# Optimization experiments

Measured on AMD Instinct MI355X. Metric: run time of the kernel, lower is better.

## Reference

```python
import jax, jax.numpy as jnp
import numpy as np

N, E, D, H, O, G = 50000, 800000, 64, 64, 32, 64


def setup_inputs() -> dict:
    key = jax.random.key(0)
    ks = jax.random.split(key, 12)
    x = jax.random.normal(ks[0], (N, D), dtype=jnp.float32)
    edge_index = jax.random.randint(ks[1], (2, E), 0, N)
    batch = jnp.sort(jax.random.randint(ks[2], (N,), 0, G))

    def glorot(k, fan_in, fan_out):
        s = np.sqrt(6.0 / (fan_in + fan_out)).astype(np.float32)
        return jax.random.uniform(k, (fan_in, fan_out), jnp.float32, -s, s)

    return {
        "x": x,
        "edge_index": edge_index,
        "batch": batch,
        "W1": glorot(ks[3], D, H), "b1": jnp.zeros((H,), jnp.float32),
        "W2": glorot(ks[4], H, H), "b2": jnp.zeros((H,), jnp.float32),
        "W3": glorot(ks[5], H, H), "b3": jnp.zeros((H,), jnp.float32),
        "Wl": glorot(ks[6], H, O), "bl": jnp.zeros((O,), jnp.float32),
    }


def reference(x, edge_index, batch, W1, b1, W2, b2, W3, b3, Wl, bl):
    n = x.shape[0]
    # GCNConv default: add self-loops, symmetric deg^-1/2 normalization
    loop = jnp.arange(n, dtype=edge_index.dtype)
    src = jnp.concatenate([edge_index[0], loop])  # [E+N]
    dst = jnp.concatenate([edge_index[1], loop])
    deg = jax.ops.segment_sum(jnp.ones_like(src, dtype=x.dtype), dst, num_segments=n)
    dis = jax.lax.rsqrt(deg)  # deg >= 1 due to self-loops
    norm = (dis[src] * dis[dst])[:, None]  # [E+N, 1]

    def gcn(h, W, b):
        hw = h @ W                      # [N, H] small GEMM
        msg = hw[src] * norm            # gather + scale: [E+N, H]
        agg = jax.ops.segment_sum(msg, dst, num_segments=n)  # scatter-add
        return agg + b

    h = jax.nn.relu(gcn(x, W1, b1))
    h = jax.nn.relu(gcn(h, W2, b2))
    h = gcn(h, W3, b3)

    # global_mean_pool over graph ids
    counts = jax.ops.segment_sum(jnp.ones((n,), h.dtype), batch, num_segments=G)
    pooled = jax.ops.segment_sum(h, batch, num_segments=G) / counts[:, None]

    # dropout(p=0.5) is identity in eval mode
    return pooled @ Wl + bl
```

## Files before the change

kernel.cpp:

```cpp
#include <hip/hip_runtime.h>

#define HD 64
#define PSUB 16
#define NBLK 256
#define LOG_NBLK 8
#define NBKT 512

__device__ __forceinline__ unsigned short f2bf(float f) {
    union { float f; unsigned u; } v; v.f = f;
    unsigned r = v.u + 0x7FFF + ((v.u >> 16) & 1);
    return (unsigned short)(r >> 16);
}
__device__ __forceinline__ float u2f(unsigned u) {
    union { unsigned u; float f; } v; v.u = u;
    return v.f;
}


__global__ __launch_bounds__(256) void hist1_k(const int* __restrict__ dst,
                                               int* __restrict__ hist, int E, int chunk)
{
    __shared__ int lh[NBKT];
    int t = threadIdx.x;
    for (int i = t; i < NBKT; i += 256) lh[i] = 0;
    __syncthreads();
    int base = blockIdx.x * chunk;
    int end  = min(base + chunk, E);
    for (int i = base + t; i < end; i += 256)
        atomicAdd(&lh[dst[i] >> 7], 1);
    __syncthreads();
    for (int i = t; i < NBKT; i += 256)
        hist[blockIdx.x * NBKT + i] = lh[i];
}

__global__ __launch_bounds__(256) void scanA_k(const int* __restrict__ hist,
                                               int* __restrict__ tsum)
{
    __shared__ int s[256];
    int t = threadIdx.x;
    int l = blockIdx.x * 256 + t;
    int phys = (l & (NBLK - 1)) * NBKT + (l >> LOG_NBLK);
    s[t] = hist[phys];
    __syncthreads();
    for (int off = 128; off > 0; off >>= 1) {
        if (t < off) s[t] += s[t + off];
        __syncthreads();
    }
    if (t == 0) tsum[blockIdx.x] = s[0];
}

__global__ __launch_bounds__(1024) void scanB_k(int* __restrict__ tsum, int nb,
    const int* __restrict__ batch, int* __restrict__ gstart, int n, int G,
    float* __restrict__ partial, int psz)
{
    __shared__ int s[1024];
    int t = threadIdx.x;
    int v = (t < nb) ? tsum[t] : 0;
    s[t] = v;
    __syncthreads();
    for (int off = 1; off < 1024; off <<= 1) {
        int u = (t >= off) ? s[t - off] : 0;
        __syncthreads();
        s[t] += u;
        __syncthreads();
    }
    if (t < nb) tsum[t] = s[t] - v;
    if (t <= G) {
        if (t == G) gstart[t] = n;
        else {
            int lo = 0, hi = n;
            while (lo < hi) { int m = (lo + hi) >> 1; if (batch[m] < t) lo = m + 1; else hi = m; }
            gstart[t] = lo;
        }
    }
    for (int i = t; i < psz; i += 1024) partial[i] = 0.f;
}

__global__ __launch_bounds__(256) void scanC_k(const int* __restrict__ hist,
                                               const int* __restrict__ tsum,
                                               int* __restrict__ scanned)
{
    __shared__ int s[256];
    int t = threadIdx.x;
    int l = blockIdx.x * 256 + t;
    int phys = (l & (NBLK - 1)) * NBKT + (l >> LOG_NBLK);
    int own = hist[phys];
    s[t] = own;
    __syncthreads();
    for (int off = 1; off < 256; off <<= 1) {
        int u = (t >= off) ? s[t - off] : 0;
        __syncthreads();
        s[t] += u;
        __syncthreads();
    }
    scanned[l] = tsum[blockIdx.x] + s[t] - own;
}

__global__ __launch_bounds__(256) void append_k(const int* __restrict__ src,
    const int* __restrict__ dst, const int* __restrict__ scanned,
    int* __restrict__ pairs, int E, int chunk)
{
    __shared__ int cur[NBKT];
    int t = threadIdx.x;
    int blk = blockIdx.x;
    for (int i = t; i < NBKT; i += 256) cur[i] = scanned[i * NBLK + blk];
    __syncthreads();
    int base = blk * chunk;
    int end  = min(base + chunk, E);
    for (int i = base + t; i < end; i += 256) {
        int s = src[i], d = dst[i];
        int p = atomicAdd(&cur[d >> 7], 1);
        pairs[p] = (s << 7) | (d & 127);
    }
}

__global__ __launch_bounds__(256) void bucket_csr_k(const int* __restrict__ pairs,
    const int* __restrict__ scanned, int* __restrict__ offsets,
    float* __restrict__ dis, int* __restrict__ csr_src, int N, int E)
{
    __shared__ int cnt[128];
    __shared__ int sc[128];
    __shared__ int cur[128];
    int t = threadIdx.x;
    int b = blockIdx.x;
    int nodeBase = b * 128;
    int nNodes = min(128, N - nodeBase);
    int bBase = scanned[b * NBLK];
    int bEnd  = (b + 1 < NBKT) ? scanned[(b + 1) * NBLK] : E;

    if (t < 128) cnt[t] = 0;
    __syncthreads();
    for (int i = bBase + t; i < bEnd; i += 256)
        atomicAdd(&cnt[pairs[i] & 127], 1);
    __syncthreads();
    int myc = (t < 128) ? cnt[t] : 0;
    if (t < 128) sc[t] = myc;
    __syncthreads();
    for (int off = 1; off < 128; off <<= 1) {
        int u = (t < 128 && t >= off) ? sc[t - off] : 0;
        __syncthreads();
        if (t < 128) sc[t] += u;
        __syncthreads();
    }
    if (t < 128) {
        int excl = sc[t] - myc;
        cur[t] = excl;
        if (t < nNodes) {
            offsets[nodeBase + t] = bBase + excl;
            dis[nodeBase + t] = rsqrtf(1.0f + (float)myc);
        }
    }
    if (t == 0 && b == gridDim.x - 1) offsets[N] = E;
    __syncthreads();
    for (int i = bBase + t; i < bEnd; i += 256) {
        int pk = pairs[i];
        int pos = bBase + atomicAdd(&cur[pk & 127], 1);
        csr_src[pos] = ((unsigned)pk) >> 7;
    }
}


__global__ __launch_bounds__(256) void gemm64_k(
    const float* __restrict__ in, const float* __restrict__ b_prev, int relu_prev,
    const float* __restrict__ W, const float* __restrict__ dis,
    unsigned short* __restrict__ outb, int n)
{
    __shared__ float HsT[HD][68];
    __shared__ float Ws[HD][HD];
    int t = threadIdx.x;
    int rowBase = blockIdx.x * 64;

    for (int i = t; i < HD * HD / 4; i += 256)
        ((float4*)Ws)[i] = ((const float4*)W)[i];

    if (blockIdx.x == 0 && t < 64)
        outb[(size_t)n * HD + t] = 0;

    {
        int k0 = (t & 15) * 4;
        float4 bb = make_float4(0.f, 0.f, 0.f, 0.f);
        if (b_prev) bb = *(const float4*)&b_prev[k0];
        for (int it = 0; it < 4; ++it) {
            int r = (t >> 4) + it * 16;
            int row = rowBase + r;
            float4 v = make_float4(0.f, 0.f, 0.f, 0.f);
            if (row < n) {
                v = *(const float4*)&in[(size_t)row * HD + k0];
                v.x += bb.x; v.y += bb.y; v.z += bb.z; v.w += bb.w;
                if (relu_prev) {
                    v.x = fmaxf(v.x, 0.f); v.y = fmaxf(v.y, 0.f);
                    v.z = fmaxf(v.z, 0.f); v.w = fmaxf(v.w, 0.f);
                }
            }
            HsT[k0 + 0][r] = v.x;
            HsT[k0 + 1][r] = v.y;
            HsT[k0 + 2][r] = v.z;
            HsT[k0 + 3][r] = v.w;
        }
    }
    __syncthreads();

    int c4 = (t & 15) * 4;
    int r4 = (t >> 4) * 4;
    float acc[4][4];
    #pragma unroll
    for (int i = 0; i < 4; ++i)
        #pragma unroll
        for (int j = 0; j < 4; ++j) acc[i][j] = 0.f;

    #pragma unroll 8
    for (int k = 0; k < HD; ++k) {
        float4 a = *(const float4*)&HsT[k][r4];
        float4 b = *(const float4*)&Ws[k][c4];
        acc[0][0] += a.x * b.x; acc[0][1] += a.x * b.y; acc[0][2] += a.x * b.z; acc[0][3] += a.x * b.w;
        acc[1][0] += a.y * b.x; acc[1][1] += a.y * b.y; acc[1][2] += a.y * b.z; acc[1][3] += a.y * b.w;
        acc[2][0] += a.z * b.x; acc[2][1] += a.z * b.y; acc[2][2] += a.z * b.z; acc[2][3] += a.z * b.w;
        acc[3][0] += a.w * b.x; acc[3][1] += a.w * b.y; acc[3][2] += a.w * b.z; acc[3][3] += a.w * b.w;
    }

    #pragma unroll
    for (int i = 0; i < 4; ++i) {
        int row = rowBase + r4 + i;
        if (row < n) {
            float ds = dis[row];
            ushort4 o;
            o.x = f2bf(ds * acc[i][0]); o.y = f2bf(ds * acc[i][1]);
            o.z = f2bf(ds * acc[i][2]); o.w = f2bf(ds * acc[i][3]);
            *(ushort4*)&outb[(size_t)row * HD + c4] = o;
        }
    }
}

__device__ __forceinline__ void gather4(const unsigned short* __restrict__ hwb,
    const int* __restrict__ offsets, const int* __restrict__ csr_src,
    int node, bool act, int n, int sub, int fl,
    float& a0, float& a1, float& a2, float& a3)
{
    int beg = 0, end = 0;
    if (act) { beg = offsets[node]; end = offsets[node + 1]; }
    int deg = end - beg;
    int md = deg;
    md = max(md, __shfl_xor(md, 16, 64));
    md = max(md, __shfl_xor(md, 32, 64));

    int nodeC = act ? node : n;
    uint2 sv = *(const uint2*)(hwb + ((size_t)nodeC << 6) + (fl << 2));
    a0 = u2f(sv.x << 16); a1 = u2f(sv.x & 0xFFFF0000u);
    a2 = u2f(sv.y << 16); a3 = u2f(sv.y & 0xFFFF0000u);

    int base = sub << 4;
    for (int jb = 0; jb < md; jb += 16) {
        int e = jb + fl;
        int idxv = (e < deg) ? csr_src[beg + e] : n;
        {
            uint2 g[8];
            #pragma unroll
            for (int j = 0; j < 8; ++j) {
                int row = __shfl(idxv, base + j, 64);
                g[j] = *(const uint2*)(hwb + ((size_t)row << 6) + (fl << 2));
            }
            #pragma unroll
            for (int j = 0; j < 8; ++j) {
                a0 += u2f(g[j].x << 16); a1 += u2f(g[j].x & 0xFFFF0000u);
                a2 += u2f(g[j].y << 16); a3 += u2f(g[j].y & 0xFFFF0000u);
            }
        }
        if (jb + 8 < md) {
            uint2 g[8];
            #pragma unroll
            for (int j = 0; j < 8; ++j) {
                int row = __shfl(idxv, base + 8 + j, 64);
                g[j] = *(const uint2*)(hwb + ((size_t)row << 6) + (fl << 2));
            }
            #pragma unroll
            for (int j = 0; j < 8; ++j) {
                a0 += u2f(g[j].x << 16); a1 += u2f(g[j].x & 0xFFFF0000u);
                a2 += u2f(g[j].y << 16); a3 += u2f(g[j].y & 0xFFFF0000u);
            }
        }
    }
}

__global__ __launch_bounds__(256) void agg4_k(const unsigned short* __restrict__ hwb,
    const float* __restrict__ dis, const int* __restrict__ offsets,
    const int* __restrict__ csr_src, float* __restrict__ agg, int n)
{
    int t    = threadIdx.x;
    int lane = t & 63;
    int sub  = lane >> 4;
    int fl   = lane & 15;
    int node = blockIdx.x * 16 + (t >> 6) * 4 + sub;
    bool act = node < n;

    float a0, a1, a2, a3;
    gather4(hwb, offsets, csr_src, node, act, n, sub, fl, a0, a1, a2, a3);

    if (act) {
        float ds = dis[node];
        *(float4*)&agg[(size_t)node * HD + (fl << 2)] =
            make_float4(a0 * ds, a1 * ds, a2 * ds, a3 * ds);
    }
}

__global__ __launch_bounds__(256) void agg_pool4_k(const unsigned short* __restrict__ hwb,
    const float* __restrict__ dis, const int* __restrict__ offsets,
    const int* __restrict__ csr_src, const int* __restrict__ batch,
    float* __restrict__ partial, int n)
{
    __shared__ float sh[16][68];
    __shared__ int gids[16];
    __shared__ int allsame;
    int t    = threadIdx.x;
    int lane = t & 63;
    int sub  = lane >> 4;
    int fl   = lane & 15;
    int w    = t >> 6;
    int nib  = w * 4 + sub;
    int node = blockIdx.x * 16 + nib;
    bool act = node < n;

    float a0, a1, a2, a3;
    gather4(hwb, offsets, csr_src, node, act, n, sub, fl, a0, a1, a2, a3);

    float ds = act ? dis[node] : 0.f;
    *(float4*)&sh[nib][fl << 2] = make_float4(a0 * ds, a1 * ds, a2 * ds, a3 * ds);
    if (fl == 0) gids[nib] = act ? batch[node] : -1;
    __syncthreads();

    if (t == 0) {
        int g0 = gids[0];
        int ok = (g0 >= 0);
        #pragma unroll
        for (int r = 1; r < 16; ++r) ok &= (gids[r] == g0);
        allsame = ok;
    }
    __syncthreads();

    int slot = blockIdx.x & (PSUB - 1);
    if (allsame) {
        if (t < 64) {
            float s = 0.f;
            #pragma unroll
            for (int r = 0; r < 16; ++r) s += sh[r][t];
            atomicAdd(&partial[((size_t)gids[0] * PSUB + slot) * HD + t], s);
        }
    } else {
        int c  = t & 63;
        int r0 = w * 4;
        int ga = gids[r0], gb = gids[r0 + 1], gc = gids[r0 + 2], gd = gids[r0 + 3];
        if (ga == gb && gb == gc && gc == gd && ga >= 0) {
            float v = sh[r0][c] + sh[r0 + 1][c] + sh[r0 + 2][c] + sh[r0 + 3][c];
            atomicAdd(&partial[((size_t)ga * PSUB + slot) * HD + c], v);
        } else {
            if (ga >= 0) atomicAdd(&partial[((size_t)ga * PSUB + slot) * HD + c], sh[r0][c]);
            if (gb >= 0) atomicAdd(&partial[((size_t)gb * PSUB + slot) * HD + c], sh[r0 + 1][c]);
            if (gc >= 0) atomicAdd(&partial[((size_t)gc * PSUB + slot) * HD + c], sh[r0 + 2][c]);
            if (gd >= 0) atomicAdd(&partial[((size_t)gd * PSUB + slot) * HD + c], sh[r0 + 3][c]);
        }
    }
}

__global__ __launch_bounds__(64) void pool2_k(const float* __restrict__ partial,
    const int* __restrict__ gstart, const float* __restrict__ b3,
    const float* __restrict__ Wl, const float* __restrict__ bl,
    float* __restrict__ out, int O)
{
    __shared__ float pooled[HD];
    int g = blockIdx.x;
    int t = threadIdx.x;
    float sum = 0.0f;
    #pragma unroll
    for (int s = 0; s < PSUB; ++s)
        sum += partial[((size_t)g * PSUB + s) * HD + t];
    float cnt = (float)(gstart[g + 1] - gstart[g]);
    pooled[t] = sum / cnt + b3[t];
    __syncthreads();
    if (t < O) {
        float acc = bl[t];
        #pragma unroll
        for (int k = 0; k < HD; ++k) acc += pooled[k] * Wl[k * O + t];
        out[g * O + t] = acc;
    }
}

extern "C" void kernel_launch(void* const* d_in, const int* in_sizes, int n_in,
                              void* d_out, int out_size, void* d_ws, size_t ws_size,
                              hipStream_t stream)
{
    const float* x    = (const float*)d_in[0];
    const int*   ei   = (const int*)d_in[1];
    const int*   batch= (const int*)d_in[2];
    const float* W1   = (const float*)d_in[3];
    const float* b1   = (const float*)d_in[4];
    const float* W2   = (const float*)d_in[5];
    const float* b2   = (const float*)d_in[6];
    const float* W3   = (const float*)d_in[7];
    const float* b3   = (const float*)d_in[8];
    const float* Wl   = (const float*)d_in[9];
    const float* bl   = (const float*)d_in[10];
    float* out = (float*)d_out;

    const int N = in_sizes[0] / HD;
    const int E = in_sizes[1] / 2;
    const int O = in_sizes[10];
    const int G = out_size / O;

    const int* src = ei;
    const int* dst = ei + E;

    char* p = (char*)d_ws;
    auto take = [&](size_t bytes) { char* r = p; p += (bytes + 255) & ~(size_t)255; return r; };
    int*   csr_src = (int*)  take((size_t)(E + 256) * 4);
    int*   offsets = (int*)  take((size_t)(N + 1) * 4);
    float* dis     = (float*)take((size_t)N * 4);
    int*   gstart  = (int*)  take((size_t)(G + 1) * 4);
    float* partial = (float*)take((size_t)G * PSUB * HD * 4);
    float* aggF    = (float*)take((size_t)N * HD * 4);
    unsigned short* hwb = (unsigned short*)take((size_t)(N + 1) * HD * 2);

    int* hist    = (int*)aggF;
    int* scanned = hist + NBLK * NBKT;
    int* tsum    = scanned + NBLK * NBKT;
    int* pairs   = (int*)hwb;

    const int TB = 256;
    int chunk   = (E + NBLK - 1) / NBLK;
    int ntiles  = (NBLK * NBKT) / 256;
    int nb_gemm = (N + 63) / 64;
    int nb_agg4 = (N + 15) / 16;
    int nbuck   = (N + 127) / 128;
    int psz     = G * PSUB * HD;

    hist1_k<<<NBLK, TB, 0, stream>>>(dst, hist, E, chunk);
    scanA_k<<<ntiles, TB, 0, stream>>>(hist, tsum);
    scanB_k<<<1, 1024, 0, stream>>>(tsum, ntiles, batch, gstart, N, G, partial, psz);
    scanC_k<<<ntiles, TB, 0, stream>>>(hist, tsum, scanned);
    append_k<<<NBLK, TB, 0, stream>>>(src, dst, scanned, pairs, E, chunk);
    bucket_csr_k<<<nbuck, TB, 0, stream>>>(pairs, scanned, offsets, dis, csr_src, N, E);

    gemm64_k<<<nb_gemm, TB, 0, stream>>>(x, nullptr, 0, W1, dis, hwb, N);
    agg4_k<<<nb_agg4, TB, 0, stream>>>(hwb, dis, offsets, csr_src, aggF, N);

    gemm64_k<<<nb_gemm, TB, 0, stream>>>(aggF, b1, 1, W2, dis, hwb, N);
    agg4_k<<<nb_agg4, TB, 0, stream>>>(hwb, dis, offsets, csr_src, aggF, N);

    gemm64_k<<<nb_gemm, TB, 0, stream>>>(aggF, b2, 1, W3, dis, hwb, N);
    agg_pool4_k<<<nb_agg4, TB, 0, stream>>>(hwb, dis, offsets, csr_src, batch, partial, N);

    pool2_k<<<G, 64, 0, stream>>>(partial, gstart, b3, Wl, bl, out, O);
}
```

Measured before the change: 209.6 us.

## Fuse aggregation with next-layer GEMM and ping-pong bf16 feature buffers

Merges each layer's neighbor aggregation with the following layer's bias, ReLU, 64x64 GEMM and dis scaling into one kernel. The aggregated 16-node tile stays in shared memory instead of round-tripping through a full-precision N x 64 buffer, which removes two kernel launches and that write/read traffic. Two bf16 buffers alternate between layers, and zeroing of the pooling partials moves from the single-block scan kernel into the histogram kernel. Each block now reloads W (16 KB) into shared memory for only 16 nodes, and the larger shared footprint may lower occupancy of the latency-bound gather.

Measured after the change: 192.4 us. 8.2% less time.

```diff
diff --git a/kernel.cpp b/kernel.cpp
--- a/kernel.cpp
+++ b/kernel.cpp
@@ -18,11 +18,14 @@
 
 
 __global__ __launch_bounds__(256) void hist1_k(const int* __restrict__ dst,
-                                               int* __restrict__ hist, int E, int chunk)
+                                               int* __restrict__ hist, int E, int chunk,
+                                               float* __restrict__ partial, int psz)
 {
     __shared__ int lh[NBKT];
     int t = threadIdx.x;
     for (int i = t; i < NBKT; i += 256) lh[i] = 0;
+    for (int i = blockIdx.x * 256 + t; i < psz; i += gridDim.x * 256)
+        partial[i] = 0.f;
     __syncthreads();
     int base = blockIdx.x * chunk;
     int end  = min(base + chunk, E);
@@ -50,8 +53,7 @@
 }
 
 __global__ __launch_bounds__(1024) void scanB_k(int* __restrict__ tsum, int nb,
-    const int* __restrict__ batch, int* __restrict__ gstart, int n, int G,
-    float* __restrict__ partial, int psz)
+    const int* __restrict__ batch, int* __restrict__ gstart, int n, int G)
 {
     __shared__ int s[1024];
     int t = threadIdx.x;
@@ -73,7 +75,6 @@
             gstart[t] = lo;
         }
     }
-    for (int i = t; i < psz; i += 1024) partial[i] = 0.f;
 }
 
 __global__ __launch_bounds__(256) void scanC_k(const int* __restrict__ hist,
@@ -281,24 +282,66 @@
     }
 }
 
-__global__ __launch_bounds__(256) void agg4_k(const unsigned short* __restrict__ hwb,
-    const float* __restrict__ dis, const int* __restrict__ offsets,
-    const int* __restrict__ csr_src, float* __restrict__ agg, int n)
-{
+__global__ __launch_bounds__(256) void agg_gemm_k(
+    const unsigned short* __restrict__ hwb, const float* __restrict__ dis,
+    const int* __restrict__ offsets, const int* __restrict__ csr_src,
+    const float* __restrict__ b_prev, const float* __restrict__ W,
+    unsigned short* __restrict__ outb, int n)
+{
+    __shared__ float As[16][68];
+    __shared__ float Ws[HD][HD];
     int t    = threadIdx.x;
     int lane = t & 63;
     int sub  = lane >> 4;
     int fl   = lane & 15;
-    int node = blockIdx.x * 16 + (t >> 6) * 4 + sub;
+    int w    = t >> 6;
+    int nib  = w * 4 + sub;
+    int nodeBase = blockIdx.x * 16;
+    int node = nodeBase + nib;
     bool act = node < n;
+
+    for (int i = t; i < HD * HD / 4; i += 256)
+        ((float4*)Ws)[i] = ((const float4*)W)[i];
+
+    if (blockIdx.x == 0 && t < 64)
+        outb[(size_t)n * HD + t] = 0;
 
     float a0, a1, a2, a3;
     gather4(hwb, offsets, csr_src, node, act, n, sub, fl, a0, a1, a2, a3);
 
-    if (act) {
-        float ds = dis[node];
-        *(float4*)&agg[(size_t)node * HD + (fl << 2)] =
-            make_float4(a0 * ds, a1 * ds, a2 * ds, a3 * ds);
+    float ds = act ? dis[node] : 0.f;
+    int c0 = fl << 2;
+    float4 bb = *(const float4*)&b_prev[c0];
+    float4 v;
+    v.x = fmaxf(a0 * ds + bb.x, 0.f);
+    v.y = fmaxf(a1 * ds + bb.y, 0.f);
+    v.z = fmaxf(a2 * ds + bb.z, 0.f);
+    v.w = fmaxf(a3 * ds + bb.w, 0.f);
+    *(float4*)&As[nib][c0] = v;
+    __syncthreads();
+
+    int r  = t & 15;
+    int c4 = (t >> 4) << 2;
+    float acc0 = 0.f, acc1 = 0.f, acc2 = 0.f, acc3 = 0.f;
+    #pragma unroll 4
+    for (int k = 0; k < HD; k += 4) {
+        float4 a  = *(const float4*)&As[r][k];
+        float4 w0 = *(const float4*)&Ws[k + 0][c4];
+        float4 w1 = *(const float4*)&Ws[k + 1][c4];
+        float4 w2 = *(const float4*)&Ws[k + 2][c4];
+        float4 w3 = *(const float4*)&Ws[k + 3][c4];
+        acc0 += a.x * w0.x + a.y * w1.x + a.z * w2.x + a.w * w3.x;
+        acc1 += a.x * w0.y + a.y * w1.y + a.z * w2.y + a.w * w3.y;
+        acc2 += a.x * w0.z + a.y * w1.z + a.z * w2.z + a.w * w3.z;
+        acc3 += a.x * w0.w + a.y * w1.w + a.z * w2.w + a.w * w3.w;
+    }
+    int orow = nodeBase + r;
+    if (orow < n) {
+        float d2 = dis[orow];
+        ushort4 o;
+        o.x = f2bf(d2 * acc0); o.y = f2bf(d2 * acc1);
+        o.z = f2bf(d2 * acc2); o.w = f2bf(d2 * acc3);
+        *(ushort4*)&outb[(size_t)orow * HD + c4] = o;
     }
 }
 
@@ -415,13 +458,13 @@
     float* dis     = (float*)take((size_t)N * 4);
     int*   gstart  = (int*)  take((size_t)(G + 1) * 4);
     float* partial = (float*)take((size_t)G * PSUB * HD * 4);
-    float* aggF    = (float*)take((size_t)N * HD * 4);
-    unsigned short* hwb = (unsigned short*)take((size_t)(N + 1) * HD * 2);
-
-    int* hist    = (int*)aggF;
+    unsigned short* hwb  = (unsigned short*)take((size_t)(N + 1) * HD * 2);
+    unsigned short* hwb2 = (unsigned short*)take((size_t)(N + 1) * HD * 2);
+
+    int* pairs   = (int*)hwb;
+    int* hist    = (int*)hwb2;
     int* scanned = hist + NBLK * NBKT;
     int* tsum    = scanned + NBLK * NBKT;
-    int* pairs   = (int*)hwb;
 
     const int TB = 256;
     int chunk   = (E + NBLK - 1) / NBLK;
@@ -431,20 +474,19 @@
     int nbuck   = (N + 127) / 128;
     int psz     = G * PSUB * HD;
 
-    hist1_k<<<NBLK, TB, 0, stream>>>(dst, hist, E, chunk);
+    hist1_k<<<NBLK, TB, 0, stream>>>(dst, hist, E, chunk, partial, psz);
     scanA_k<<<ntiles, TB, 0, stream>>>(hist, tsum);
-    scanB_k<<<1, 1024, 0, stream>>>(tsum, ntiles, batch, gstart, N, G, partial, psz);
+    scanB_k<<<1, 1024, 0, stream>>>(tsum, ntiles, batch, gstart, N, G);
     scanC_k<<<ntiles, TB, 0, stream>>>(hist, tsum, scanned);
     append_k<<<NBLK, TB, 0, stream>>>(src, dst, scanned, pairs, E, chunk);
     bucket_csr_k<<<nbuck, TB, 0, stream>>>(pairs, scanned, offsets, dis, csr_src, N, E);
 
     gemm64_k<<<nb_gemm, TB, 0, stream>>>(x, nullptr, 0, W1, dis, hwb, N);
-    agg4_k<<<nb_agg4, TB, 0, stream>>>(hwb, dis, offsets, csr_src, aggF, N);
-
-    gemm64_k<<<nb_gemm, TB, 0, stream>>>(aggF, b1, 1, W2, dis, hwb, N);
-    agg4_k<<<nb_agg4, TB, 0, stream>>>(hwb, dis, offsets, csr_src, aggF, N);
-
-    gemm64_k<<<nb_gemm, TB, 0, stream>>>(aggF, b2, 1, W3, dis, hwb, N);
+
+    agg_gemm_k<<<nb_agg4, TB, 0, stream>>>(hwb, dis, offsets, csr_src, b1, W2, hwb2, N);
+
+    agg_gemm_k<<<nb_agg4, TB, 0, stream>>>(hwb2, dis, offsets, csr_src, b2, W3, hwb, N);
+
     agg_pool4_k<<<nb_agg4, TB, 0, stream>>>(hwb, dis, offsets, csr_src, batch, partial, N);
 
     pool2_k<<<G, 64, 0, stream>>>(partial, gstart, b3, Wl, bl, out, O);
```

## Split neighbor aggregation into feature halves with four-lane node groups

Applied to the files above, without the earlier changes.

Replaces the 16-lane-per-node gather with 4 lanes per node over one 32-feature half, using 16-byte loads. Each block handles 64 nodes, and blocks are interleaved so the two halves of nearby node blocks run close together. The edge-index load for the next step is issued one iteration ahead, using nontemporal loads and stores. The partial-buffer zeroing moves into the histogram kernel, and a second hw buffer alternates between layers. More lanes stay busy on low-degree nodes, at the cost of more divergence across the max-degree loop and more atomics in the pool kernel.

Result: slower. 227.9 us (+8.8%).

```diff
diff --git a/kernel.cpp b/kernel.cpp
--- a/kernel.cpp
+++ b/kernel.cpp
@@ -6,6 +6,8 @@
 #define LOG_NBLK 8
 #define NBKT 512
 
+typedef float f32x4 __attribute__((ext_vector_type(4)));
+
 __device__ __forceinline__ unsigned short f2bf(float f) {
     union { float f; unsigned u; } v; v.f = f;
     unsigned r = v.u + 0x7FFF + ((v.u >> 16) & 1);
@@ -18,11 +20,14 @@
 
 
 __global__ __launch_bounds__(256) void hist1_k(const int* __restrict__ dst,
-                                               int* __restrict__ hist, int E, int chunk)
+                                               int* __restrict__ hist, int E, int chunk,
+                                               float* __restrict__ partial, int psz)
 {
     __shared__ int lh[NBKT];
     int t = threadIdx.x;
     for (int i = t; i < NBKT; i += 256) lh[i] = 0;
+    for (int i = blockIdx.x * 256 + t; i < psz; i += gridDim.x * 256)
+        partial[i] = 0.f;
     __syncthreads();
     int base = blockIdx.x * chunk;
     int end  = min(base + chunk, E);
@@ -50,8 +55,7 @@
 }
 
 __global__ __launch_bounds__(1024) void scanB_k(int* __restrict__ tsum, int nb,
-    const int* __restrict__ batch, int* __restrict__ gstart, int n, int G,
-    float* __restrict__ partial, int psz)
+    const int* __restrict__ batch, int* __restrict__ gstart, int n, int G)
 {
     __shared__ int s[1024];
     int t = threadIdx.x;
@@ -73,7 +77,6 @@
             gstart[t] = lo;
         }
     }
-    for (int i = t; i < psz; i += 1024) partial[i] = 0.f;
 }
 
 __global__ __launch_bounds__(256) void scanC_k(const int* __restrict__ hist,
@@ -231,99 +234,113 @@
     }
 }
 
-__device__ __forceinline__ void gather4(const unsigned short* __restrict__ hwb,
+__device__ __forceinline__ void gather_half(const unsigned short* __restrict__ hwb,
     const int* __restrict__ offsets, const int* __restrict__ csr_src,
-    int node, bool act, int n, int sub, int fl,
-    float& a0, float& a1, float& a2, float& a3)
+    int node, bool act, int n, int lane, int fl, int eoff, float* a )
 {
     int beg = 0, end = 0;
     if (act) { beg = offsets[node]; end = offsets[node + 1]; }
     int deg = end - beg;
     int md = deg;
+    md = max(md, __shfl_xor(md, 4, 64));
+    md = max(md, __shfl_xor(md, 8, 64));
     md = max(md, __shfl_xor(md, 16, 64));
     md = max(md, __shfl_xor(md, 32, 64));
 
     int nodeC = act ? node : n;
-    uint2 sv = *(const uint2*)(hwb + ((size_t)nodeC << 6) + (fl << 2));
-    a0 = u2f(sv.x << 16); a1 = u2f(sv.x & 0xFFFF0000u);
-    a2 = u2f(sv.y << 16); a3 = u2f(sv.y & 0xFFFF0000u);
-
-    int base = sub << 4;
-    for (int jb = 0; jb < md; jb += 16) {
-        int e = jb + fl;
-        int idxv = (e < deg) ? csr_src[beg + e] : n;
-        {
-            uint2 g[8];
-            #pragma unroll
-            for (int j = 0; j < 8; ++j) {
-                int row = __shfl(idxv, base + j, 64);
-                g[j] = *(const uint2*)(hwb + ((size_t)row << 6) + (fl << 2));
-            }
-            #pragma unroll
-            for (int j = 0; j < 8; ++j) {
-                a0 += u2f(g[j].x << 16); a1 += u2f(g[j].x & 0xFFFF0000u);
-                a2 += u2f(g[j].y << 16); a3 += u2f(g[j].y & 0xFFFF0000u);
-            }
-        }
-        if (jb + 8 < md) {
-            uint2 g[8];
-            #pragma unroll
-            for (int j = 0; j < 8; ++j) {
-                int row = __shfl(idxv, base + 8 + j, 64);
-                g[j] = *(const uint2*)(hwb + ((size_t)row << 6) + (fl << 2));
-            }
-            #pragma unroll
-            for (int j = 0; j < 8; ++j) {
-                a0 += u2f(g[j].x << 16); a1 += u2f(g[j].x & 0xFFFF0000u);
-                a2 += u2f(g[j].y << 16); a3 += u2f(g[j].y & 0xFFFF0000u);
-            }
-        }
-    }
-}
-
-__global__ __launch_bounds__(256) void agg4_k(const unsigned short* __restrict__ hwb,
-    const float* __restrict__ dis, const int* __restrict__ offsets,
-    const int* __restrict__ csr_src, float* __restrict__ agg, int n)
-{
+    uint4 sv = *(const uint4*)(hwb + ((size_t)nodeC << 6) + eoff);
+    a[0] = u2f(sv.x << 16); a[1] = u2f(sv.x & 0xFFFF0000u);
+    a[2] = u2f(sv.y << 16); a[3] = u2f(sv.y & 0xFFFF0000u);
+    a[4] = u2f(sv.z << 16); a[5] = u2f(sv.z & 0xFFFF0000u);
+    a[6] = u2f(sv.w << 16); a[7] = u2f(sv.w & 0xFFFF0000u);
+
+    int grpbase = lane & 60;
+    int idxv = (fl < deg) ? __builtin_nontemporal_load(csr_src + beg + fl) : n;
+    for (int jb = 0; jb < md; jb += 4) {
+        int e2 = jb + 4 + fl;
+        int nidx = (e2 < deg) ? __builtin_nontemporal_load(csr_src + beg + e2) : n;
+        uint4 g[4];
+        #pragma unroll
+        for (int j = 0; j < 4; ++j) {
+            int row = __shfl(idxv, grpbase + j, 64);
+            g[j] = *(const uint4*)(hwb + ((size_t)row << 6) + eoff);
+        }
+        #pragma unroll
+        for (int j = 0; j < 4; ++j) {
+            a[0] += u2f(g[j].x << 16); a[1] += u2f(g[j].x & 0xFFFF0000u);
+            a[2] += u2f(g[j].y << 16); a[3] += u2f(g[j].y & 0xFFFF0000u);
+            a[4] += u2f(g[j].z << 16); a[5] += u2f(g[j].z & 0xFFFF0000u);
+            a[6] += u2f(g[j].w << 16); a[7] += u2f(g[j].w & 0xFFFF0000u);
+        }
+        idxv = nidx;
+    }
+}
+
+__global__ __launch_bounds__(256) void agg_half_k(
+    const unsigned short* __restrict__ hwb, const float* __restrict__ dis,
+    const int* __restrict__ offsets, const int* __restrict__ csr_src,
+    float* __restrict__ aggF, int n, int nblocks)
+{
+    int bid = blockIdx.x;
+    int r8  = bid & 7;
+    int h   = r8 >> 2;
+    int nbi = (bid >> 3) * 4 + (r8 & 3);
+    if (nbi >= nblocks) return;
+
     int t    = threadIdx.x;
     int lane = t & 63;
-    int sub  = lane >> 4;
-    int fl   = lane & 15;
-    int node = blockIdx.x * 16 + (t >> 6) * 4 + sub;
+    int grp  = lane >> 2;
+    int fl   = lane & 3;
+    int w    = t >> 6;
+    int nib  = w * 16 + grp;
+    int node = nbi * 64 + nib;
     bool act = node < n;
-
-    float a0, a1, a2, a3;
-    gather4(hwb, offsets, csr_src, node, act, n, sub, fl, a0, a1, a2, a3);
+    int eoff = (h << 5) + (fl << 3);
+
+    float a[8];
+    gather_half(hwb, offsets, csr_src, node, act, n, lane, fl, eoff, a);
 
     if (act) {
         float ds = dis[node];
-        *(float4*)&agg[(size_t)node * HD + (fl << 2)] =
-            make_float4(a0 * ds, a1 * ds, a2 * ds, a3 * ds);
-    }
-}
-
-__global__ __launch_bounds__(256) void agg_pool4_k(const unsigned short* __restrict__ hwb,
-    const float* __restrict__ dis, const int* __restrict__ offsets,
-    const int* __restrict__ csr_src, const int* __restrict__ batch,
-    float* __restrict__ partial, int n)
-{
-    __shared__ float sh[16][68];
-    __shared__ int gids[16];
+        f32x4 o0 = { a[0] * ds, a[1] * ds, a[2] * ds, a[3] * ds };
+        f32x4 o1 = { a[4] * ds, a[5] * ds, a[6] * ds, a[7] * ds };
+        __builtin_nontemporal_store(o0, (f32x4*)&aggF[(size_t)node * HD + eoff]);
+        __builtin_nontemporal_store(o1, (f32x4*)&aggF[(size_t)node * HD + eoff + 4]);
+    }
+}
+
+__global__ __launch_bounds__(256) void agg_pool_half_k(
+    const unsigned short* __restrict__ hwb, const float* __restrict__ dis,
+    const int* __restrict__ offsets, const int* __restrict__ csr_src,
+    const int* __restrict__ batch, float* __restrict__ partial, int n, int nblocks)
+{
+    __shared__ float sh[64][36];
+    __shared__ int gids[64];
     __shared__ int allsame;
+    int bid = blockIdx.x;
+    int r8  = bid & 7;
+    int h   = r8 >> 2;
+    int nbi = (bid >> 3) * 4 + (r8 & 3);
+    if (nbi >= nblocks) return;
+
     int t    = threadIdx.x;
     int lane = t & 63;
-    int sub  = lane >> 4;
-    int fl   = lane & 15;
+    int grp  = lane >> 2;
+    int fl   = lane & 3;
     int w    = t >> 6;
-    int nib  = w * 4 + sub;
-    int node = blockIdx.x * 16 + nib;
+    int nib  = w * 16 + grp;
+    int node = nbi * 64 + nib;
     bool act = node < n;
-
-    float a0, a1, a2, a3;
-    gather4(hwb, offsets, csr_src, node, act, n, sub, fl, a0, a1, a2, a3);
+    int hoff = h << 5;
+    int eoff = hoff + (fl << 3);
+
+    float a[8];
+    gather_half(hwb, offsets, csr_src, node, act, n, lane, fl, eoff, a);
 
     float ds = act ? dis[node] : 0.f;
-    *(float4*)&sh[nib][fl << 2] = make_float4(a0 * ds, a1 * ds, a2 * ds, a3 * ds);
+    int cl0 = fl << 3;
+    *(float4*)&sh[nib][cl0]     = make_float4(a[0] * ds, a[1] * ds, a[2] * ds, a[3] * ds);
+    *(float4*)&sh[nib][cl0 + 4] = make_float4(a[4] * ds, a[5] * ds, a[6] * ds, a[7] * ds);
     if (fl == 0) gids[nib] = act ? batch[node] : -1;
     __syncthreads();
 
@@ -331,31 +348,29 @@
         int g0 = gids[0];
         int ok = (g0 >= 0);
         #pragma unroll
-        for (int r = 1; r < 16; ++r) ok &= (gids[r] == g0);
+        for (int r = 1; r < 64; ++r) ok &= (gids[r] == g0);
         allsame = ok;
     }
     __syncthreads();
 
-    int slot = blockIdx.x & (PSUB - 1);
+    int slot = bid & (PSUB - 1);
     if (allsame) {
-        if (t < 64) {
+        if (t < 32) {
             float s = 0.f;
             #pragma unroll
-            for (int r = 0; r < 16; ++r) s += sh[r][t];
-            atomicAdd(&partial[((size_t)gids[0] * PSUB + slot) * HD + t], s);
+            for (int rr = 0; rr < 64; ++rr) s += sh[rr][t];
+            atomicAdd(&partial[((size_t)gids[0] * PSUB + slot) * HD + hoff + t], s);
         }
     } else {
-        int c  = t & 63;
-        int r0 = w * 4;
-        int ga = gids[r0], gb = gids[r0 + 1], gc = gids[r0 + 2], gd = gids[r0 + 3];
-        if (ga == gb && gb == gc && gc == gd && ga >= 0) {
-            float v = sh[r0][c] + sh[r0 + 1][c] + sh[r0 + 2][c] + sh[r0 + 3][c];
-            atomicAdd(&partial[((size_t)ga * PSUB + slot) * HD + c], v);
-        } else {
-            if (ga >= 0) atomicAdd(&partial[((size_t)ga * PSUB + slot) * HD + c], sh[r0][c]);
-            if (gb >= 0) atomicAdd(&partial[((size_t)gb * PSUB + slot) * HD + c], sh[r0 + 1][c]);
-            if (gc >= 0) atomicAdd(&partial[((size_t)gc * PSUB + slot) * HD + c], sh[r0 + 2][c]);
-            if (gd >= 0) atomicAdd(&partial[((size_t)gd * PSUB + slot) * HD + c], sh[r0 + 3][c]);
+        int r0 = w * 16;
+        if (lane < 32) {
+            int c = lane;
+            for (int rr = 0; rr < 16; ++rr) {
+                int gg = gids[r0 + rr];
+                if (gg >= 0)
+                    atomicAdd(&partial[((size_t)gg * PSUB + slot) * HD + hoff + c],
+                              sh[r0 + rr][c]);
+            }
         }
     }
 }
@@ -416,36 +431,41 @@
     int*   gstart  = (int*)  take((size_t)(G + 1) * 4);
     float* partial = (float*)take((size_t)G * PSUB * HD * 4);
     float* aggF    = (float*)take((size_t)N * HD * 4);
-    unsigned short* hwb = (unsigned short*)take((size_t)(N + 1) * HD * 2);
-
+    unsigned short* hwb  = (unsigned short*)take((size_t)(N + 1) * HD * 2);
+    unsigned short* hwb2 = (unsigned short*)take((size_t)(N + 1) * HD * 2);
+
+    int* pairs   = (int*)hwb;
     int* hist    = (int*)aggF;
     int* scanned = hist + NBLK * NBKT;
     int* tsum    = scanned + NBLK * NBKT;
-    int* pairs   = (int*)hwb;
 
     const int TB = 256;
     int chunk   = (E + NBLK - 1) / NBLK;
     int ntiles  = (NBLK * NBKT) / 256;
     int nb_gemm = (N + 63) / 64;
-    int nb_agg4 = (N + 15) / 16;
+    int nblocks = (N + 63) / 64;
+    int nbq     = (nblocks + 3) / 4;
+    int nb_aggh = nbq * 8;
     int nbuck   = (N + 127) / 128;
     int psz     = G * PSUB * HD;
 
-    hist1_k<<<NBLK, TB, 0, stream>>>(dst, hist, E, chunk);
+    hist1_k<<<NBLK, TB, 0, stream>>>(dst, hist, E, chunk, partial, psz);
     scanA_k<<<ntiles, TB, 0, stream>>>(hist, tsum);
-    scanB_k<<<1, 1024, 0, stream>>>(tsum, ntiles, batch, gstart, N, G, partial, psz);
+    scanB_k<<<1, 1024, 0, stream>>>(tsum, ntiles, batch, gstart, N, G);
     scanC_k<<<ntiles, TB, 0, stream>>>(hist, tsum, scanned);
     append_k<<<NBLK, TB, 0, stream>>>(src, dst, scanned, pairs, E, chunk);
     bucket_csr_k<<<nbuck, TB, 0, stream>>>(pairs, scanned, offsets, dis, csr_src, N, E);
 
     gemm64_k<<<nb_gemm, TB, 0, stream>>>(x, nullptr, 0, W1, dis, hwb, N);
-    agg4_k<<<nb_agg4, TB, 0, stream>>>(hwb, dis, offsets, csr_src, aggF, N);
-
-    gemm64_k<<<nb_gemm, TB, 0, stream>>>(aggF, b1, 1, W2, dis, hwb, N);
-    agg4_k<<<nb_agg4, TB, 0, stream>>>(hwb, dis, offsets, csr_src, aggF, N);
-
+
+    agg_half_k<<<nb_aggh, TB, 0, stream>>>(hwb, dis, offsets, csr_src, aggF, N, nblocks);
+    gemm64_k<<<nb_gemm, TB, 0, stream>>>(aggF, b1, 1, W2, dis, hwb2, N);
+
+    agg_half_k<<<nb_aggh, TB, 0, stream>>>(hwb2, dis, offsets, csr_src, aggF, N, nblocks);
     gemm64_k<<<nb_gemm, TB, 0, stream>>>(aggF, b2, 1, W3, dis, hwb, N);
-    agg_pool4_k<<<nb_agg4, TB, 0, stream>>>(hwb, dis, offsets, csr_src, batch, partial, N);
+
+    agg_pool_half_k<<<nb_aggh, TB, 0, stream>>>(hwb, dis, offsets, csr_src, batch,
+                                                partial, N, nblocks);
 
     pool2_k<<<G, 64, 0, stream>>>(partial, gstart, b3, Wl, bl, out, O);
 }
```
